# Optimization experiments

Hardware: AMD Instinct MI355X
Metric: run time of the kernel (lower is better)

Reference implementation:

```python
import jax, jax.numpy as jnp
import numpy as np

# Config constants (match init_kwargs / config)
B = 16        # config.BATCH_SIZE
T = 2048      # config.TRAIN_LEN
C = 256       # input channels (input_shape[-1])
K = 8         # kernel_size
F = 256       # nb_filters
DIL = 4       # dilation_rate


def setup_inputs() -> dict:
    key = jax.random.key(0)
    k1, k2, k3 = jax.random.split(key, 3)
    inputs = jax.random.normal(k1, (B, T, C), dtype=jnp.float32)
    kernel = jax.random.normal(k2, (C, K, F), dtype=jnp.float32) * 0.05
    bias = jax.random.normal(k3, (F,), dtype=jnp.float32) * 0.05
    return {"inputs": inputs, "kernel": kernel, "bias": bias}


def reference(inputs, kernel, bias):
    # Original TF layer computes, per (b,t,k,f):
    #   raw[b,t,k,f] = sum_c (x[b,t,c] * kernel[c,k,f] + bias[f])
    #               = conv[b,t,k,f] + C * bias[f]
    # (bias is added BEFORE the reduce_sum over the channel axis, so it is
    #  scaled by C — we reproduce that quirk faithfully.)
    # Then each (t,k) slice is scatter-added to output time t + k*dilation
    # (the gather_nd + zero-pad construction in TF implements exactly this
    #  dilated transposed-conv scatter; non-matching positions gather zeros),
    # and finally the last T timesteps are kept.
    Bq, Tq, Cq = inputs.shape
    Kq, Fq = kernel.shape[1], kernel.shape[2]
    conv = jnp.einsum('btc,ckf->btkf', inputs, kernel) + jnp.asarray(Cq, inputs.dtype) * bias
    L = Tq + (Kq - 1) * DIL  # final_time_len
    # scatter positions: out[i + j*DIL] += conv[:, i, j, :]
    pos = (jnp.arange(Tq)[:, None] + DIL * jnp.arange(Kq)[None, :]).reshape(-1)  # (T*K,)
    out = jnp.zeros((Bq, L, Fq), dtype=conv.dtype)
    out = out.at[:, pos, :].add(conv.reshape(Bq, Tq * Kq, Fq))
    return out[:, -Tq:, :]
```

## Files before the change

kernel.cpp:

```cpp
#include <hip/hip_runtime.h>
#include <hip/hip_bf16.h>


#define B_    16
#define T_    2048
#define C_    256
#define KT    8
#define F_    256
#define SH    28
#define BT    128
#define ROWS  (BT + SH)
#define CH    32
#define LSTR  40
#define CHUNK (ROWS * LSTR)

typedef __attribute__((ext_vector_type(8))) short short8;
typedef __attribute__((ext_vector_type(4))) float floatx4;

__global__ __launch_bounds__(256) void wprep_kernel(const float* __restrict__ W,
                                                    ushort* __restrict__ Wf) {
    const int tid  = threadIdx.x;
    const int fid  = blockIdx.x * 4 + (tid >> 6);
    const int lane = tid & 63;
    const int g    = fid & 15;
    const int j    = (fid >> 4) & 7;
    const int cs   = fid >> 7;
    const int c0   = cs * 32 + (lane >> 4) * 8;
    const int f    = g * 16 + (lane & 15);
    short8 pk;
    #pragma unroll
    for (int i = 0; i < 8; ++i) {
        __hip_bfloat16 h = __float2bfloat16(W[((c0 + i) * KT + j) * F_ + f]);
        pk[i] = *reinterpret_cast<const short*>(&h);
    }
    *reinterpret_cast<short8*>(Wf + fid * 512 + lane * 8) = pk;
}

__device__ inline short8 cvt8(float4 a, float4 b) {
    float v[8] = {a.x, a.y, a.z, a.w, b.x, b.y, b.z, b.w};
    short8 r;
    #pragma unroll
    for (int i = 0; i < 8; ++i) {
        __hip_bfloat16 h = __float2bfloat16(v[i]);
        r[i] = *reinterpret_cast<const short*>(&h);
    }
    return r;
}

__global__ __launch_bounds__(512, 2) void deconv_kernel(
        const float* __restrict__ x, const ushort* __restrict__ Wf,
        const float* __restrict__ bias, float* __restrict__ out) {
    __shared__ ushort xs[2 * CHUNK];
    const int t0   = blockIdx.x * BT;
    const int b    = blockIdx.y;
    const int tid  = threadIdx.x;
    const int lane = tid & 63, wave = tid >> 6;
    const int l16  = lane & 15, q = lane >> 4;

    const int r0  = tid >> 2,  qd0 = tid & 3;
    const int idx1 = tid + 512;
    const int r1  = idx1 >> 2, qd1 = idx1 & 3;

    float4 R[2][2];

#define STAGE_LOAD(cs_) do {                                                   \
        R[0][0] = make_float4(0,0,0,0); R[0][1] = make_float4(0,0,0,0);        \
        R[1][0] = make_float4(0,0,0,0); R[1][1] = make_float4(0,0,0,0);        \
        if (t0 + r0 < T_) {                                                    \
            const float4* p = reinterpret_cast<const float4*>(                 \
                x + ((size_t)(b * T_ + t0 + r0) * C_ + (cs_) * CH + qd0 * 8)); \
            R[0][0] = p[0]; R[0][1] = p[1];                                    \
        }                                                                      \
        if (idx1 < ROWS * 4 && t0 + r1 < T_) {                                 \
            const float4* p = reinterpret_cast<const float4*>(                 \
                x + ((size_t)(b * T_ + t0 + r1) * C_ + (cs_) * CH + qd1 * 8)); \
            R[1][0] = p[0]; R[1][1] = p[1];                                    \
        } } while (0)

#define STAGE_WRITE(buf_) do {                                                 \
        ushort* d_ = xs + (buf_) * CHUNK;                                      \
        *reinterpret_cast<short8*>(d_ + r0 * LSTR + qd0 * 8) =                 \
            cvt8(R[0][0], R[0][1]);                                            \
        if (idx1 < ROWS * 4)                                                   \
            *reinterpret_cast<short8*>(d_ + r1 * LSTR + qd1 * 8) =             \
                cvt8(R[1][0], R[1][1]);                                        \
        } while (0)

    float bf2[2];
    bf2[0] = bias[wave * 32 + l16];
    bf2[1] = bias[wave * 32 + 16 + l16];

    floatx4 acc[8][2];
    #pragma unroll
    for (int mf = 0; mf < 8; ++mf) {
        acc[mf][0] = (floatx4){0.f, 0.f, 0.f, 0.f};
        acc[mf][1] = (floatx4){0.f, 0.f, 0.f, 0.f};
    }

    const ushort* wb = Wf + (wave * 2) * 512 + lane * 8;

#define LOAD_A(buf_, j_, arr) do {                                             \
        const ushort* s_ = xs + (buf_) * CHUNK                                 \
                           + (l16 + (SH - 4 * (j_))) * LSTR + q * 8;           \
        _Pragma("unroll")                                                      \
        for (int mf = 0; mf < 8; ++mf)                                         \
            arr[mf] = *reinterpret_cast<const short8*>(s_ + mf * 16 * LSTR);   \
        } while (0)

#define LOAD_B(cs_, j_, arr) do {                                              \
        const ushort* p_ = wb + (size_t)(cs_) * 65536 + (j_) * 8192;           \
        arr[0] = *reinterpret_cast<const short8*>(p_);                         \
        arr[1] = *reinterpret_cast<const short8*>(p_ + 512);                   \
        } while (0)

#define DO_MFMA(aa, bb) do {                                                   \
        _Pragma("unroll")                                                      \
        for (int mf = 0; mf < 8; ++mf) {                                       \
            acc[mf][0] = __builtin_amdgcn_mfma_f32_16x16x32_bf16(              \
                aa[mf], bb[0], acc[mf][0], 0, 0, 0);                           \
            acc[mf][1] = __builtin_amdgcn_mfma_f32_16x16x32_bf16(              \
                aa[mf], bb[1], acc[mf][1], 0, 0, 0);                           \
        } } while (0)

    STAGE_LOAD(0);
    STAGE_WRITE(0);
    __syncthreads();

    for (int cs = 0; cs < 8; ++cs) {
        const int buf = cs & 1;
        if (cs < 7) STAGE_LOAD(cs + 1);

        short8 a[2][8], bb[2][2];
        LOAD_A(buf, 0, a[0]); LOAD_B(cs, 0, bb[0]);
        LOAD_A(buf, 1, a[1]); LOAD_B(cs, 1, bb[1]);
        #pragma unroll
        for (int j = 0; j < 8; ++j) {
            DO_MFMA(a[j & 1], bb[j & 1]);
            if (j < 6) { LOAD_A(buf, j + 2, a[j & 1]); LOAD_B(cs, j + 2, bb[j & 1]); }
        }

        if (cs < 7) STAGE_WRITE(buf ^ 1);
        __syncthreads();
    }

    #pragma unroll
    for (int nf = 0; nf < 2; ++nf) {
        const int f = wave * 32 + nf * 16 + l16;
        #pragma unroll
        for (int mf = 0; mf < 8; ++mf) {
            #pragma unroll
            for (int r = 0; r < 4; ++r) {
                const int t = t0 + mf * 16 + q * 4 + r;
                const int jmin = (t < T_ - SH) ? 0 : (((t - (T_ - SH)) >> 2) + 1);
                out[(b * T_ + t) * F_ + f] =
                    acc[mf][nf][r] + (float)(8 - jmin) * 256.0f * bf2[nf];
            }
        }
    }
#undef STAGE_LOAD
#undef STAGE_WRITE
#undef LOAD_A
#undef LOAD_B
#undef DO_MFMA
}

extern "C" void kernel_launch(void* const* d_in, const int* in_sizes, int n_in,
                              void* d_out, int out_size, void* d_ws, size_t ws_size,
                              hipStream_t stream) {
    const float* x    = (const float*)d_in[0];
    const float* W    = (const float*)d_in[1];
    const float* bias = (const float*)d_in[2];
    float* out = (float*)d_out;
    ushort* Wf = (ushort*)d_ws;

    wprep_kernel<<<256, 256, 0, stream>>>(W, Wf);
    dim3 grid(T_ / BT, B_);
    deconv_kernel<<<grid, 512, 0, stream>>>(x, Wf, bias, out);
}
```

Before: 53.01 us.

## Retile waves to 4x4 MFMA fragments with 64-channel swizzled LDS chunks

Each block's 8 waves now form a 2x4 grid: every wave computes 64 timesteps by 64 filters as 4x4 MFMA fragments, instead of 128 timesteps by 32 filters. This balances A and B fragment reuse per wave. Channel chunks grow from 32 to 64, so there are 4 stages instead of 8 and fewer barriers. The LDS layout changes from padded rows to an XOR swizzle to avoid bank conflicts. Weight prefetch now runs across stage boundaries and MFMA issue is prioritised with setprio, at the cost of more register pressure and larger LDS use.

```diff
diff --git a/kernel.cpp b/kernel.cpp
--- a/kernel.cpp
+++ b/kernel.cpp
@@ -10,9 +10,8 @@
 #define SH    28
 #define BT    128
 #define ROWS  (BT + SH)
-#define CH    32
-#define LSTR  40
-#define CHUNK (ROWS * LSTR)
+#define NTASK (ROWS * 8)
+#define CHW   (ROWS * 64)
 
 typedef __attribute__((ext_vector_type(8))) short short8;
 typedef __attribute__((ext_vector_type(4))) float floatx4;
@@ -23,9 +22,9 @@
     const int fid  = blockIdx.x * 4 + (tid >> 6);
     const int lane = tid & 63;
     const int g    = fid & 15;
-    const int j    = (fid >> 4) & 7;
-    const int cs   = fid >> 7;
-    const int c0   = cs * 32 + (lane >> 4) * 8;
+    const int S    = fid >> 4;
+    const int kh   = S & 1, j = (S >> 1) & 7, cs = S >> 4;
+    const int c0   = cs * 64 + kh * 32 + (lane >> 4) * 8;
     const int f    = g * 16 + (lane & 15);
     short8 pk;
     #pragma unroll
@@ -33,7 +32,7 @@
         __hip_bfloat16 h = __float2bfloat16(W[((c0 + i) * KT + j) * F_ + f]);
         pk[i] = *reinterpret_cast<const short*>(&h);
     }
-    *reinterpret_cast<short8*>(Wf + fid * 512 + lane * 8) = pk;
+    *reinterpret_cast<short8*>(Wf + (size_t)fid * 512 + lane * 8) = pk;
 }
 
 __device__ inline short8 cvt8(float4 a, float4 b) {
@@ -50,110 +49,127 @@
 __global__ __launch_bounds__(512, 2) void deconv_kernel(
         const float* __restrict__ x, const ushort* __restrict__ Wf,
         const float* __restrict__ bias, float* __restrict__ out) {
-    __shared__ ushort xs[2 * CHUNK];
+    __shared__ ushort xs[2 * CHW];
     const int t0   = blockIdx.x * BT;
     const int b    = blockIdx.y;
     const int tid  = threadIdx.x;
-    const int lane = tid & 63, wave = tid >> 6;
+    const int lane = tid & 63, w = tid >> 6;
+    const int wf   = w & 3, wm = w >> 2;
     const int l16  = lane & 15, q = lane >> 4;
 
-    const int r0  = tid >> 2,  qd0 = tid & 3;
-    const int idx1 = tid + 512;
-    const int r1  = idx1 >> 2, qd1 = idx1 & 3;
+    const int r0 = tid >> 3,          g0 = tid & 7;
+    const int r1 = (tid + 512) >> 3,  g1 = tid & 7;
+    const int r2 = (tid + 1024) >> 3, g2 = tid & 7;
 
-    float4 R[2][2];
+    float4 A0, B0, A1, B1, A2, B2;
 
 #define STAGE_LOAD(cs_) do {                                                   \
-        R[0][0] = make_float4(0,0,0,0); R[0][1] = make_float4(0,0,0,0);        \
-        R[1][0] = make_float4(0,0,0,0); R[1][1] = make_float4(0,0,0,0);        \
-        if (t0 + r0 < T_) {                                                    \
-            const float4* p = reinterpret_cast<const float4*>(                 \
-                x + ((size_t)(b * T_ + t0 + r0) * C_ + (cs_) * CH + qd0 * 8)); \
-            R[0][0] = p[0]; R[0][1] = p[1];                                    \
-        }                                                                      \
-        if (idx1 < ROWS * 4 && t0 + r1 < T_) {                                 \
-            const float4* p = reinterpret_cast<const float4*>(                 \
-                x + ((size_t)(b * T_ + t0 + r1) * C_ + (cs_) * CH + qd1 * 8)); \
-            R[1][0] = p[0]; R[1][1] = p[1];                                    \
+        const float4 z_ = make_float4(0.f, 0.f, 0.f, 0.f);                     \
+        A0 = z_; B0 = z_; A1 = z_; B1 = z_; A2 = z_; B2 = z_;                  \
+        {   const float4* p_ = reinterpret_cast<const float4*>(                \
+                x + ((size_t)(b * T_ + t0 + r0) * C_ + (cs_) * 64 + g0 * 8));  \
+            A0 = p_[0]; B0 = p_[1]; }                                          \
+        {   const float4* p_ = reinterpret_cast<const float4*>(                \
+                x + ((size_t)(b * T_ + t0 + r1) * C_ + (cs_) * 64 + g1 * 8));  \
+            A1 = p_[0]; B1 = p_[1]; }                                          \
+        if (tid < 224 && t0 + r2 < T_) {                                       \
+            const float4* p_ = reinterpret_cast<const float4*>(                \
+                x + ((size_t)(b * T_ + t0 + r2) * C_ + (cs_) * 64 + g2 * 8));  \
+            A2 = p_[0]; B2 = p_[1]; } } while (0)
+
+#define STAGE_WRITE(buf_) do {                                                 \
+        ushort* d_ = xs + (buf_) * CHW;                                        \
+        *reinterpret_cast<short8*>(d_ + r0 * 64 + ((g0 ^ (r0 & 7)) * 8)) =     \
+            cvt8(A0, B0);                                                      \
+        *reinterpret_cast<short8*>(d_ + r1 * 64 + ((g1 ^ (r1 & 7)) * 8)) =     \
+            cvt8(A1, B1);                                                      \
+        if (tid < 224)                                                         \
+            *reinterpret_cast<short8*>(d_ + r2 * 64 + ((g2 ^ (r2 & 7)) * 8)) = \
+                cvt8(A2, B2);                                                  \
+        } while (0)
+
+#define LOAD_A(buf_, s_, arr) do {                                             \
+        const int j_ = (s_) >> 1, kh_ = (s_) & 1;                              \
+        const int rb_ = SH - 4 * j_ + wm * 64 + l16;                           \
+        _Pragma("unroll")                                                      \
+        for (int mf = 0; mf < 4; ++mf) {                                       \
+            const int row_ = rb_ + mf * 16;                                    \
+            arr[mf] = *reinterpret_cast<const short8*>(                        \
+                xs + (buf_) * CHW + row_ * 64 +                                \
+                (((kh_ * 4 + q) ^ (row_ & 7)) * 8));                           \
         } } while (0)
 
-#define STAGE_WRITE(buf_) do {                                                 \
-        ushort* d_ = xs + (buf_) * CHUNK;                                      \
-        *reinterpret_cast<short8*>(d_ + r0 * LSTR + qd0 * 8) =                 \
-            cvt8(R[0][0], R[0][1]);                                            \
-        if (idx1 < ROWS * 4)                                                   \
-            *reinterpret_cast<short8*>(d_ + r1 * LSTR + qd1 * 8) =             \
-                cvt8(R[1][0], R[1][1]);                                        \
-        } while (0)
-
-    float bf2[2];
-    bf2[0] = bias[wave * 32 + l16];
-    bf2[1] = bias[wave * 32 + 16 + l16];
-
-    floatx4 acc[8][2];
-    #pragma unroll
-    for (int mf = 0; mf < 8; ++mf) {
-        acc[mf][0] = (floatx4){0.f, 0.f, 0.f, 0.f};
-        acc[mf][1] = (floatx4){0.f, 0.f, 0.f, 0.f};
-    }
-
-    const ushort* wb = Wf + (wave * 2) * 512 + lane * 8;
-
-#define LOAD_A(buf_, j_, arr) do {                                             \
-        const ushort* s_ = xs + (buf_) * CHUNK                                 \
-                           + (l16 + (SH - 4 * (j_))) * LSTR + q * 8;           \
+#define LOAD_B(S_, arr) do {                                                   \
+        const ushort* p_ = wbase + (size_t)(S_) * 8192;                        \
         _Pragma("unroll")                                                      \
-        for (int mf = 0; mf < 8; ++mf)                                         \
-            arr[mf] = *reinterpret_cast<const short8*>(s_ + mf * 16 * LSTR);   \
-        } while (0)
-
-#define LOAD_B(cs_, j_, arr) do {                                              \
-        const ushort* p_ = wb + (size_t)(cs_) * 65536 + (j_) * 8192;           \
-        arr[0] = *reinterpret_cast<const short8*>(p_);                         \
-        arr[1] = *reinterpret_cast<const short8*>(p_ + 512);                   \
+        for (int nf = 0; nf < 4; ++nf)                                         \
+            arr[nf] = *reinterpret_cast<const short8*>(p_ + nf * 512);         \
         } while (0)
 
 #define DO_MFMA(aa, bb) do {                                                   \
         _Pragma("unroll")                                                      \
-        for (int mf = 0; mf < 8; ++mf) {                                       \
-            acc[mf][0] = __builtin_amdgcn_mfma_f32_16x16x32_bf16(              \
-                aa[mf], bb[0], acc[mf][0], 0, 0, 0);                           \
-            acc[mf][1] = __builtin_amdgcn_mfma_f32_16x16x32_bf16(              \
-                aa[mf], bb[1], acc[mf][1], 0, 0, 0);                           \
-        } } while (0)
+        for (int mf = 0; mf < 4; ++mf)                                         \
+            _Pragma("unroll")                                                  \
+            for (int nf = 0; nf < 4; ++nf)                                     \
+                acc[mf][nf] = __builtin_amdgcn_mfma_f32_16x16x32_bf16(         \
+                    aa[mf], bb[nf], acc[mf][nf], 0, 0, 0);                     \
+        } while (0)
+
+    const ushort* wbase = Wf + wf * 2048 + (size_t)lane * 8;
+
+    float bf4[4];
+    #pragma unroll
+    for (int nf = 0; nf < 4; ++nf) bf4[nf] = bias[wf * 64 + nf * 16 + l16];
+
+    floatx4 acc[4][4];
+    #pragma unroll
+    for (int mf = 0; mf < 4; ++mf)
+        #pragma unroll
+        for (int nf = 0; nf < 4; ++nf)
+            acc[mf][nf] = (floatx4){0.f, 0.f, 0.f, 0.f};
+
+    short8 aA[4], aB[4], bA[4], bB[4];
 
     STAGE_LOAD(0);
+    LOAD_B(0, bA);
+    LOAD_B(1, bB);
     STAGE_WRITE(0);
     __syncthreads();
 
-    for (int cs = 0; cs < 8; ++cs) {
+    for (int cs = 0; cs < 4; ++cs) {
         const int buf = cs & 1;
-        if (cs < 7) STAGE_LOAD(cs + 1);
-
-        short8 a[2][8], bb[2][2];
-        LOAD_A(buf, 0, a[0]); LOAD_B(cs, 0, bb[0]);
-        LOAD_A(buf, 1, a[1]); LOAD_B(cs, 1, bb[1]);
+        if (cs < 3) STAGE_LOAD(cs + 1);
+        LOAD_A(buf, 0, aA);
+        LOAD_A(buf, 1, aB);
         #pragma unroll
-        for (int j = 0; j < 8; ++j) {
-            DO_MFMA(a[j & 1], bb[j & 1]);
-            if (j < 6) { LOAD_A(buf, j + 2, a[j & 1]); LOAD_B(cs, j + 2, bb[j & 1]); }
+        for (int s = 0; s < 16; s += 2) {
+            const int S = cs * 16 + s;
+            __builtin_amdgcn_s_setprio(1);
+            DO_MFMA(aA, bA);
+            __builtin_amdgcn_s_setprio(0);
+            if (s < 14) LOAD_A(buf, s + 2, aA);
+            LOAD_B((S + 2) & 63, bA);
+            __builtin_amdgcn_s_setprio(1);
+            DO_MFMA(aB, bB);
+            __builtin_amdgcn_s_setprio(0);
+            if (s < 14) LOAD_A(buf, s + 3, aB);
+            LOAD_B((S + 3) & 63, bB);
         }
-
-        if (cs < 7) STAGE_WRITE(buf ^ 1);
+        if (cs < 3) STAGE_WRITE(buf ^ 1);
         __syncthreads();
     }
 
     #pragma unroll
-    for (int nf = 0; nf < 2; ++nf) {
-        const int f = wave * 32 + nf * 16 + l16;
+    for (int mf = 0; mf < 4; ++mf) {
         #pragma unroll
-        for (int mf = 0; mf < 8; ++mf) {
+        for (int nf = 0; nf < 4; ++nf) {
+            const int f = wf * 64 + nf * 16 + l16;
             #pragma unroll
             for (int r = 0; r < 4; ++r) {
-                const int t = t0 + mf * 16 + q * 4 + r;
+                const int t = t0 + wm * 64 + mf * 16 + q * 4 + r;
                 const int jmin = (t < T_ - SH) ? 0 : (((t - (T_ - SH)) >> 2) + 1);
-                out[(b * T_ + t) * F_ + f] =
-                    acc[mf][nf][r] + (float)(8 - jmin) * 256.0f * bf2[nf];
+                out[(size_t)(b * T_ + t) * F_ + f] =
+                    acc[mf][nf][r] + (float)(8 - jmin) * 256.0f * bf4[nf];
             }
         }
     }
```

Measured after the change: 45.23 us. 14.7% less time.
